# Optimization experiments

Measured on AMD Instinct MI355X. Metric: run time of the kernel, lower is better.

Reference implementation:

```python
import jax, jax.numpy as jnp
import numpy as np

CHEB_K = 3
DIM_IN = 2
HIDDEN = 64
EMBED_DIM = 10
NODE_NUM = 2048
BATCH = 32


def _gconv(x, supports, W, b, cheb_k=CHEB_K):
    # Chebyshev graph conv applied directly to x (equivalent to building
    # T_k(A) matrices then applying: T_k(A) x = 2 A T_{k-1}(A) x - T_{k-2}(A) x).
    xs = [x, jnp.einsum('nm,bmc->bnc', supports, x)]
    for _ in range(2, cheb_k):
        xs.append(2.0 * jnp.einsum('nm,bmc->bnc', supports, xs[-1]) - xs[-2])
    x_g = jnp.concatenate(xs, axis=-1)          # [B, N, cheb_k*C]
    return jnp.einsum('bni,io->bno', x_g, W) + b


def setup_inputs() -> dict:
    key = jax.random.key(0)
    ks = jax.random.split(key, 7)
    c_in = DIM_IN + HIDDEN                       # 66
    # xavier_normal-ish scale for weights
    def xavier(k, fan_in, fan_out):
        std = float(np.sqrt(2.0 / (fan_in + fan_out)))
        return jax.random.normal(k, (fan_in, fan_out), dtype=jnp.float32) * std
    return {
        'x': jax.random.normal(ks[0], (BATCH, NODE_NUM, DIM_IN), dtype=jnp.float32),
        'state': jax.random.normal(ks[1], (BATCH, NODE_NUM, HIDDEN), dtype=jnp.float32),
        'node_embeddings': jax.random.normal(ks[2], (NODE_NUM, EMBED_DIM), dtype=jnp.float32),
        'W_gate': xavier(ks[3], CHEB_K * c_in, 2 * HIDDEN),
        'b_gate': jnp.zeros((2 * HIDDEN,), dtype=jnp.float32),
        'W_update': xavier(ks[4], CHEB_K * c_in, HIDDEN),
        'b_update': jnp.zeros((HIDDEN,), dtype=jnp.float32),
    }


def reference(x, state, node_embeddings, W_gate, b_gate, W_update, b_update):
    # adaptive adjacency: softmax(relu(E E^T), axis=1)
    logits = jnp.einsum('nc,mc->nm', node_embeddings, node_embeddings)
    supports = jax.nn.softmax(jax.nn.relu(logits), axis=1)   # [N, N]

    input_and_state = jnp.concatenate([x, state], axis=-1)   # [B, N, dim_in+hidden]
    z_r = jax.nn.sigmoid(_gconv(input_and_state, supports, W_gate, b_gate))
    z, r = jnp.split(z_r, 2, axis=-1)                        # each [B, N, hidden]
    candidate = jnp.concatenate([x, z * state], axis=-1)
    hc = jnp.tanh(_gconv(candidate, supports, W_update, b_update))
    h = r * state + (1.0 - r) * hc
    return h
```

## Files before the change

### kernel.cpp

```cpp
#include <hip/hip_runtime.h>


typedef __bf16 bf16x8 __attribute__((ext_vector_type(8)));
typedef __bf16 bf16x4 __attribute__((ext_vector_type(4)));
typedef float  f32x4  __attribute__((ext_vector_type(4)));

#define GLB(p) ((__attribute__((address_space(1))) void*)(void*)(p))
#define LDS(p) ((__attribute__((address_space(3))) void*)(p))

__global__ void supports_kernel(const float* __restrict__ E, __bf16* __restrict__ S) {
    const int n = blockIdx.x;
    const int t = threadIdx.x;
    const int l = t & 63, w = t >> 6;
    float en[10];
#pragma unroll
    for (int i = 0; i < 10; ++i) en[i] = E[n * 10 + i];
    float vals[8];
    float mx = 0.f;
#pragma unroll
    for (int q = 0; q < 8; ++q) {
        const int m = q * 256 + t;
        const float* em = E + (size_t)m * 10;
        float d = 0.f;
#pragma unroll
        for (int i = 0; i < 10; ++i) d += en[i] * em[i];
        d = fmaxf(d, 0.f);
        vals[q] = d;
        mx = fmaxf(mx, d);
    }
#pragma unroll
    for (int off = 32; off; off >>= 1) mx = fmaxf(mx, __shfl_xor(mx, off));
    __shared__ float sm[4], ss[4];
    if (l == 0) sm[w] = mx;
    __syncthreads();
    mx = fmaxf(fmaxf(sm[0], sm[1]), fmaxf(sm[2], sm[3]));
    float sum = 0.f;
#pragma unroll
    for (int q = 0; q < 8; ++q) { vals[q] = __expf(vals[q] - mx); sum += vals[q]; }
#pragma unroll
    for (int off = 32; off; off >>= 1) sum += __shfl_xor(sum, off);
    if (l == 0) ss[w] = sum;
    __syncthreads();
    sum = ss[0] + ss[1] + ss[2] + ss[3];
    const float inv = 1.f / sum;
#pragma unroll
    for (int q = 0; q < 8; ++q) S[(size_t)n * 2048 + q * 256 + t] = (__bf16)(vals[q] * inv);
}

__global__ __launch_bounds__(256, 2)
void build_t2(const float* __restrict__ x, const float* __restrict__ st,
              const __bf16* __restrict__ zr, __bf16* __restrict__ T) {
    __shared__ float Ls[66 * 129];
    const int b  = blockIdx.x >> 4;
    const int n0 = (blockIdx.x & 15) << 7;
    const int t = threadIdx.x;
    const size_t mb = (size_t)b * 2048 + n0;
    if (t < 128) {
        const float2 v = *(const float2*)&x[(mb + t) * 2];
        Ls[t] = v.x;
        Ls[129 + t] = v.y;
    }
#pragma unroll
    for (int r = 0; r < 8; ++r) {
        const int task = r * 256 + t;
        const int q = task & 15, n = task >> 4;
        f32x4 v = *(const f32x4*)&st[(mb + n) * 64 + q * 4];
        if (zr) {
            const bf16x4 z = *(const bf16x4*)&zr[(mb + n) * 128 + q * 4];
#pragma unroll
            for (int j = 0; j < 4; ++j) v[j] *= (float)z[j];
        }
        const int base = (2 + q * 4) * 129 + n;
#pragma unroll
        for (int j = 0; j < 4; ++j) Ls[base + j * 129] = v[j];
    }
    __syncthreads();
#pragma unroll
    for (int r = 0; r < 5; ++r) {
        const int task = r * 256 + t;
        if (task < 1056) {
            const int c = task >> 4, seg = task & 15;
            const float* src = &Ls[c * 129 + seg * 8];
            bf16x8 o;
#pragma unroll
            for (int j = 0; j < 8; ++j) o[j] = (__bf16)src[j];
            *(bf16x8*)&T[(size_t)(b * 66 + c) * 2048 + n0 + seg * 8] = o;
        }
    }
}

__global__ __launch_bounds__(256, 2)
void transpose_g(const __bf16* __restrict__ T0, const __bf16* __restrict__ T1,
                 const __bf16* __restrict__ T2, __bf16* __restrict__ G) {
    __shared__ __bf16 Ls[128 * 256];
    const int b  = blockIdx.x >> 4;
    const int n0 = (blockIdx.x & 15) << 7;
    const int t = threadIdx.x;
#pragma unroll
    for (int r = 0; r < 16; ++r) {
        const int task = r * 256 + t;
        const int k = task >> 4, seg = task & 15;
        bf16x8 v;
        if (k < 198) {
            const __bf16* T; int c;
            if (k < 66)       { T = T0; c = k; }
            else if (k < 132) { T = T1; c = k - 66; }
            else              { T = T2; c = k - 132; }
            v = *(const bf16x8*)&T[(size_t)(b * 66 + c) * 2048 + n0 + seg * 8];
        } else {
#pragma unroll
            for (int j = 0; j < 8; ++j) v[j] = (__bf16)0.f;
        }
        const int base = seg * 8 * 256 + (((k >> 3) ^ seg) << 3) + (k & 7);
#pragma unroll
        for (int j = 0; j < 8; ++j) Ls[base + j * 256] = v[j];
    }
    __syncthreads();
#pragma unroll
    for (int r = 0; r < 16; ++r) {
        const int task = r * 256 + t;
        const int m = task >> 5, c8 = task & 31;
        bf16x8 w = *(const bf16x8*)&Ls[m * 256 + ((c8 ^ (m >> 3)) << 3)];
        *(bf16x8*)&G[(size_t)(b * 2048 + n0 + m) * 256 + c8 * 8] = w;
    }
}

__global__ void build_wt(const float* __restrict__ W, __bf16* __restrict__ WT, int Nout) {
    const int id = blockIdx.x * 256 + threadIdx.x;
    const int o = id >> 8, k = id & 255;
    WT[id] = (o < Nout && k < 198) ? (__bf16)W[(size_t)k * Nout + o] : (__bf16)0.f;
}

__global__ __launch_bounds__(256, 3)
void gemm_pipe(const __bf16* __restrict__ A, int lda,
               const __bf16* __restrict__ Bt, int ldb,
               int K, int epi, int swz,
               __bf16* __restrict__ outT, const __bf16* __restrict__ subT,
               float* __restrict__ outF, const float* __restrict__ bias,
               __bf16* __restrict__ zrO, const __bf16* __restrict__ zrI,
               const float* __restrict__ state) {
    __shared__ __align__(16) __bf16 As[2][128 * 64];
    __shared__ __align__(16) __bf16 Bs[2][64 * 64];
    int mt, ct;
    if (swz) { mt = blockIdx.x & 15; ct = blockIdx.x >> 4; }
    else     { mt = blockIdx.x;      ct = blockIdx.y; }
    const int m0 = mt * 128, c0 = ct * 64;
    const int t = threadIdx.x;
    const int l = t & 63, w = t >> 6;
    const int wr = w >> 1, wc = w & 1;
    const int lm = l & 15, kq = l >> 4, lm7 = lm & 7;
    const int sr = l >> 3;
    const int gsw = (l & 7) ^ sr;

    f32x4 acc[4][2];
#pragma unroll
    for (int i = 0; i < 4; ++i)
#pragma unroll
        for (int j = 0; j < 2; ++j) acc[i][j] = (f32x4)0.f;

    const __bf16* Asrc = A  + (size_t)(m0 + w * 8 + sr) * lda + gsw * 8;
    const __bf16* Bsrc = Bt + (size_t)(c0 + w * 8 + sr) * ldb + gsw * 8;
    const int dstA = w * 512 + l * 8;
    const int dstB = w * 512 + l * 8;

    auto stage = [&](int buf, int k0) {
#pragma unroll
        for (int q = 0; q < 4; ++q)
            __builtin_amdgcn_global_load_lds(GLB(Asrc + (size_t)q * 32 * lda + k0),
                                             LDS(&As[buf][q * 2048 + dstA]), 16, 0, 0);
#pragma unroll
        for (int q = 0; q < 2; ++q)
            __builtin_amdgcn_global_load_lds(GLB(Bsrc + (size_t)q * 32 * ldb + k0),
                                             LDS(&Bs[buf][q * 2048 + dstB]), 16, 0, 0);
    };
    auto compute = [&](int buf) {
#pragma unroll
        for (int ks = 0; ks < 2; ++ks) {
            const int ga = (((ks << 2) | kq) ^ lm7) << 3;
            bf16x8 af[4], bfr[2];
#pragma unroll
            for (int i = 0; i < 4; ++i)
                af[i] = *(const bf16x8*)&As[buf][(wr * 64 + i * 16 + lm) * 64 + ga];
#pragma unroll
            for (int j = 0; j < 2; ++j)
                bfr[j] = *(const bf16x8*)&Bs[buf][(wc * 32 + j * 16 + lm) * 64 + ga];
#pragma unroll
            for (int i = 0; i < 4; ++i)
#pragma unroll
                for (int j = 0; j < 2; ++j)
                    acc[i][j] = __builtin_amdgcn_mfma_f32_16x16x32_bf16(af[i], bfr[j], acc[i][j], 0, 0, 0);
        }
    };

    stage(0, 0);
    const int iters = K >> 6;
    for (int i = 0; i + 2 <= iters; i += 2) {
        stage(1, (i + 1) << 6);
        __builtin_amdgcn_sched_barrier(0);
        __builtin_amdgcn_s_waitcnt(0x0F76);
        __builtin_amdgcn_s_barrier();
        __builtin_amdgcn_sched_barrier(0);
        compute(0);
        __builtin_amdgcn_sched_barrier(0);
        __builtin_amdgcn_s_barrier();
        __builtin_amdgcn_sched_barrier(0);
        if (i + 2 < iters) {
            stage(0, (i + 2) << 6);
            __builtin_amdgcn_sched_barrier(0);
            __builtin_amdgcn_s_waitcnt(0x0F76);
        } else {
            __builtin_amdgcn_s_waitcnt(0x0F70);
        }
        __builtin_amdgcn_s_barrier();
        __builtin_amdgcn_sched_barrier(0);
        compute(1);
        __builtin_amdgcn_sched_barrier(0);
        if (i + 4 <= iters) {
            __builtin_amdgcn_s_barrier();
            __builtin_amdgcn_sched_barrier(0);
        }
    }

    const int rb0 = m0 + wr * 64 + kq * 4;
    const int cb0 = c0 + wc * 32 + lm;
#pragma unroll
    for (int i = 0; i < 4; ++i) {
        const int rbase = rb0 + i * 16;
#pragma unroll
        for (int j = 0; j < 2; ++j) {
            const int c = cb0 + j * 16;
            f32x4 v = acc[i][j];
            if (epi == 0) {
                bf16x4 pk;
#pragma unroll
                for (int r = 0; r < 4; ++r) pk[r] = (__bf16)v[r];
                *(bf16x4*)&outT[(size_t)c * 2048 + rbase] = pk;
            } else if (epi == 1) {
                bf16x4 s = *(const bf16x4*)&subT[(size_t)c * 2048 + rbase];
                bf16x4 pk;
#pragma unroll
                for (int r = 0; r < 4; ++r) pk[r] = (__bf16)(2.f * v[r] - (float)s[r]);
                *(bf16x4*)&outT[(size_t)c * 2048 + rbase] = pk;
            } else if (epi == 2) {
                const float bb = bias[c];
#pragma unroll
                for (int r = 0; r < 4; ++r) {
                    float xx = fminf(fmaxf(v[r] + bb, -30.f), 30.f);
                    zrO[(size_t)(rbase + r) * 128 + c] = (__bf16)(1.f / (1.f + __expf(-xx)));
                }
            } else {
                if (c < 64) {
                    const float bb = bias[c];
#pragma unroll
                    for (int r = 0; r < 4; ++r) {
                        const int m = rbase + r;
                        float xx = fminf(fmaxf(v[r] + bb, -15.f), 15.f);
                        float e = __expf(2.f * xx);
                        float hc = (e - 1.f) / (e + 1.f);
                        float rr = (float)zrI[(size_t)m * 128 + 64 + c];
                        float s = state[(size_t)m * 64 + c];
                        outF[(size_t)m * 64 + c] = rr * s + (1.f - rr) * hc;
                    }
                }
            }
        }
    }
}

extern "C" void kernel_launch(void* const* d_in, const int* in_sizes, int n_in,
                              void* d_out, int out_size, void* d_ws, size_t ws_size,
                              hipStream_t stream) {
    (void)in_sizes; (void)n_in; (void)out_size; (void)ws_size;
    const float* x  = (const float*)d_in[0];
    const float* st = (const float*)d_in[1];
    const float* E  = (const float*)d_in[2];
    const float* Wg = (const float*)d_in[3];
    const float* bg = (const float*)d_in[4];
    const float* Wu = (const float*)d_in[5];
    const float* bu = (const float*)d_in[6];
    float* out = (float*)d_out;

    char* p = (char*)d_ws;
    __bf16* S   = (__bf16*)p; p += (size_t)2048 * 2048 * 2;
    __bf16* T0  = (__bf16*)p; p += (size_t)2112 * 2048 * 2;
    __bf16* T1  = (__bf16*)p; p += (size_t)2112 * 2048 * 2;
    __bf16* T2  = (__bf16*)p; p += (size_t)2112 * 2048 * 2;
    __bf16* G   = (__bf16*)p; p += (size_t)65536 * 256 * 2;
    __bf16* ZR  = (__bf16*)p; p += (size_t)65536 * 128 * 2;
    __bf16* WTg = (__bf16*)p; p += 128 * 256 * 2;
    __bf16* WTu = (__bf16*)p; p += 128 * 256 * 2;

    build_wt<<<128, 256, 0, stream>>>(Wg, WTg, 128);
    build_wt<<<128, 256, 0, stream>>>(Wu, WTu, 64);
    supports_kernel<<<2048, 256, 0, stream>>>(E, S);

    build_t2<<<512, 256, 0, stream>>>(x, st, nullptr, T0);
    gemm_pipe<<<528, 256, 0, stream>>>(S, 2048, T0, 2048, 2048, 0, 1, T1, nullptr, nullptr, nullptr, nullptr, nullptr, nullptr);
    gemm_pipe<<<528, 256, 0, stream>>>(S, 2048, T1, 2048, 2048, 1, 1, T2, T0, nullptr, nullptr, nullptr, nullptr, nullptr);
    transpose_g<<<512, 256, 0, stream>>>(T0, T1, T2, G);
    gemm_pipe<<<dim3(512, 2), 256, 0, stream>>>(G, 256, WTg, 256, 256, 2, 0, nullptr, nullptr, nullptr, bg, ZR, nullptr, nullptr);

    build_t2<<<512, 256, 0, stream>>>(x, st, ZR, T0);
    gemm_pipe<<<528, 256, 0, stream>>>(S, 2048, T0, 2048, 2048, 0, 1, T1, nullptr, nullptr, nullptr, nullptr, nullptr, nullptr);
    gemm_pipe<<<528, 256, 0, stream>>>(S, 2048, T1, 2048, 2048, 1, 1, T2, T0, nullptr, nullptr, nullptr, nullptr, nullptr);
    transpose_g<<<512, 256, 0, stream>>>(T0, T1, T2, G);
    gemm_pipe<<<dim3(512, 1), 256, 0, stream>>>(G, 256, WTu, 256, 256, 3, 0, nullptr, nullptr, out, bu, nullptr, ZR, st);
}
```

Measured before the change: 278.6 us.

## Write G directly from build_t2 and GEMM epilogues, drop transpose, triple-buffer GEMM

Removes the separate transpose_g kernel and T2 buffer. build_t2 and the Chebyshev GEMM epilogues now write their outputs straight into the node-major G matrix, using a padded 72-column section layout, and the weight transpose is remapped to match that layout. The goal is to avoid an extra full read and write pass over T0/T1/T2 and two kernel launches per gconv. The GEMM pipeline also moves from double to triple buffering with prefetch distance two, which uses more LDS and lowers launch bounds occupancy from 3 to 2. The new epilogue G stores are scalar and strided, so writes are less coalesced.

```diff
diff --git a/kernel.cpp b/kernel.cpp
--- a/kernel.cpp
+++ b/kernel.cpp
@@ -49,7 +49,8 @@
 
 __global__ __launch_bounds__(256, 2)
 void build_t2(const float* __restrict__ x, const float* __restrict__ st,
-              const __bf16* __restrict__ zr, __bf16* __restrict__ T) {
+              const __bf16* __restrict__ zr, __bf16* __restrict__ T,
+              __bf16* __restrict__ G) {
     __shared__ float Ls[66 * 129];
     const int b  = blockIdx.x >> 4;
     const int n0 = (blockIdx.x & 15) << 7;
@@ -87,60 +88,41 @@
             *(bf16x8*)&T[(size_t)(b * 66 + c) * 2048 + n0 + seg * 8] = o;
         }
     }
-}
-
-__global__ __launch_bounds__(256, 2)
-void transpose_g(const __bf16* __restrict__ T0, const __bf16* __restrict__ T1,
-                 const __bf16* __restrict__ T2, __bf16* __restrict__ G) {
-    __shared__ __bf16 Ls[128 * 256];
-    const int b  = blockIdx.x >> 4;
-    const int n0 = (blockIdx.x & 15) << 7;
-    const int t = threadIdx.x;
-#pragma unroll
-    for (int r = 0; r < 16; ++r) {
-        const int task = r * 256 + t;
-        const int k = task >> 4, seg = task & 15;
-        bf16x8 v;
-        if (k < 198) {
-            const __bf16* T; int c;
-            if (k < 66)       { T = T0; c = k; }
-            else if (k < 132) { T = T1; c = k - 66; }
-            else              { T = T2; c = k - 132; }
-            v = *(const bf16x8*)&T[(size_t)(b * 66 + c) * 2048 + n0 + seg * 8];
-        } else {
-#pragma unroll
-            for (int j = 0; j < 8; ++j) v[j] = (__bf16)0.f;
-        }
-        const int base = seg * 8 * 256 + (((k >> 3) ^ seg) << 3) + (k & 7);
-#pragma unroll
-        for (int j = 0; j < 8; ++j) Ls[base + j * 256] = v[j];
-    }
-    __syncthreads();
-#pragma unroll
-    for (int r = 0; r < 16; ++r) {
-        const int task = r * 256 + t;
-        const int m = task >> 5, c8 = task & 31;
-        bf16x8 w = *(const bf16x8*)&Ls[m * 256 + ((c8 ^ (m >> 3)) << 3)];
-        *(bf16x8*)&G[(size_t)(b * 2048 + n0 + m) * 256 + c8 * 8] = w;
+    {
+        const int n = t & 127, half = t >> 7;
+        const size_t grow = ((size_t)(b * 2048 + n0 + n)) * 256;
+        for (int oct = half * 5; oct < (half ? 9 : 5); ++oct) {
+            bf16x8 o8;
+#pragma unroll
+            for (int j = 0; j < 8; ++j) {
+                const int cc = oct * 8 + j;
+                o8[j] = (cc < 66) ? (__bf16)Ls[cc * 129 + n] : (__bf16)0.f;
+            }
+            *(bf16x8*)&G[grow + oct * 8] = o8;
+        }
     }
 }
 
 __global__ void build_wt(const float* __restrict__ W, __bf16* __restrict__ WT, int Nout) {
     const int id = blockIdx.x * 256 + threadIdx.x;
     const int o = id >> 8, k = id & 255;
-    WT[id] = (o < Nout && k < 198) ? (__bf16)W[(size_t)k * Nout + o] : (__bf16)0.f;
-}
-
-__global__ __launch_bounds__(256, 3)
+    const int jj = (k >= 144) ? 2 : (k >= 72 ? 1 : 0);
+    const int cc = k - 72 * jj;
+    const bool ok = (o < Nout) && (cc < 66) && (k < 216);
+    WT[id] = ok ? (__bf16)W[(size_t)(66 * jj + cc) * Nout + o] : (__bf16)0.f;
+}
+
+__global__ __launch_bounds__(256, 2)
 void gemm_pipe(const __bf16* __restrict__ A, int lda,
                const __bf16* __restrict__ Bt, int ldb,
                int K, int epi, int swz,
                __bf16* __restrict__ outT, const __bf16* __restrict__ subT,
                float* __restrict__ outF, const float* __restrict__ bias,
                __bf16* __restrict__ zrO, const __bf16* __restrict__ zrI,
-               const float* __restrict__ state) {
-    __shared__ __align__(16) __bf16 As[2][128 * 64];
-    __shared__ __align__(16) __bf16 Bs[2][64 * 64];
+               const float* __restrict__ state,
+               __bf16* __restrict__ Gout, int gsec) {
+    __shared__ __align__(16) __bf16 As[3][128 * 64];
+    __shared__ __align__(16) __bf16 Bs[3][64 * 64];
     int mt, ct;
     if (swz) { mt = blockIdx.x & 15; ct = blockIdx.x >> 4; }
     else     { mt = blockIdx.x;      ct = blockIdx.y; }
@@ -161,7 +143,6 @@
     const __bf16* Asrc = A  + (size_t)(m0 + w * 8 + sr) * lda + gsw * 8;
     const __bf16* Bsrc = Bt + (size_t)(c0 + w * 8 + sr) * ldb + gsw * 8;
     const int dstA = w * 512 + l * 8;
-    const int dstB = w * 512 + l * 8;
 
     auto stage = [&](int buf, int k0) {
 #pragma unroll
@@ -171,19 +152,21 @@
 #pragma unroll
         for (int q = 0; q < 2; ++q)
             __builtin_amdgcn_global_load_lds(GLB(Bsrc + (size_t)q * 32 * ldb + k0),
-                                             LDS(&Bs[buf][q * 2048 + dstB]), 16, 0, 0);
+                                             LDS(&Bs[buf][q * 2048 + dstA]), 16, 0, 0);
     };
     auto compute = [&](int buf) {
+        const __bf16* Ab = &As[buf][0];
+        const __bf16* Bb = &Bs[buf][0];
 #pragma unroll
         for (int ks = 0; ks < 2; ++ks) {
             const int ga = (((ks << 2) | kq) ^ lm7) << 3;
             bf16x8 af[4], bfr[2];
 #pragma unroll
             for (int i = 0; i < 4; ++i)
-                af[i] = *(const bf16x8*)&As[buf][(wr * 64 + i * 16 + lm) * 64 + ga];
+                af[i] = *(const bf16x8*)&Ab[(wr * 64 + i * 16 + lm) * 64 + ga];
 #pragma unroll
             for (int j = 0; j < 2; ++j)
-                bfr[j] = *(const bf16x8*)&Bs[buf][(wc * 32 + j * 16 + lm) * 64 + ga];
+                bfr[j] = *(const bf16x8*)&Bb[(wc * 32 + j * 16 + lm) * 64 + ga];
 #pragma unroll
             for (int i = 0; i < 4; ++i)
 #pragma unroll
@@ -193,33 +176,32 @@
     };
 
     stage(0, 0);
+    stage(1, 64);
     const int iters = K >> 6;
-    for (int i = 0; i + 2 <= iters; i += 2) {
-        stage(1, (i + 1) << 6);
-        __builtin_amdgcn_sched_barrier(0);
-        __builtin_amdgcn_s_waitcnt(0x0F76);
+    int cur = 0;
+    for (int it = 0; it < iters - 2; ++it) {
+        int pre = cur + 2; if (pre >= 3) pre -= 3;
+        stage(pre, (it + 2) << 6);
+        __builtin_amdgcn_sched_barrier(0);
+        __builtin_amdgcn_s_waitcnt(0x0F7C);
         __builtin_amdgcn_s_barrier();
         __builtin_amdgcn_sched_barrier(0);
-        compute(0);
+        compute(cur);
         __builtin_amdgcn_sched_barrier(0);
         __builtin_amdgcn_s_barrier();
         __builtin_amdgcn_sched_barrier(0);
-        if (i + 2 < iters) {
-            stage(0, (i + 2) << 6);
-            __builtin_amdgcn_sched_barrier(0);
-            __builtin_amdgcn_s_waitcnt(0x0F76);
-        } else {
-            __builtin_amdgcn_s_waitcnt(0x0F70);
-        }
-        __builtin_amdgcn_s_barrier();
-        __builtin_amdgcn_sched_barrier(0);
-        compute(1);
-        __builtin_amdgcn_sched_barrier(0);
-        if (i + 4 <= iters) {
-            __builtin_amdgcn_s_barrier();
-            __builtin_amdgcn_sched_barrier(0);
-        }
-    }
+        cur = (cur == 2) ? 0 : cur + 1;
+    }
+    __builtin_amdgcn_s_waitcnt(0x0F76);
+    __builtin_amdgcn_s_barrier();
+    __builtin_amdgcn_sched_barrier(0);
+    compute(cur);
+    cur = (cur == 2) ? 0 : cur + 1;
+    __builtin_amdgcn_sched_barrier(0);
+    __builtin_amdgcn_s_waitcnt(0x0F70);
+    __builtin_amdgcn_s_barrier();
+    __builtin_amdgcn_sched_barrier(0);
+    compute(cur);
 
     const int rb0 = m0 + wr * 64 + kq * 4;
     const int cb0 = c0 + wc * 32 + lm;
@@ -230,17 +212,21 @@
         for (int j = 0; j < 2; ++j) {
             const int c = cb0 + j * 16;
             f32x4 v = acc[i][j];
-            if (epi == 0) {
+            if (epi <= 1) {
                 bf16x4 pk;
-#pragma unroll
-                for (int r = 0; r < 4; ++r) pk[r] = (__bf16)v[r];
-                *(bf16x4*)&outT[(size_t)c * 2048 + rbase] = pk;
-            } else if (epi == 1) {
-                bf16x4 s = *(const bf16x4*)&subT[(size_t)c * 2048 + rbase];
-                bf16x4 pk;
-#pragma unroll
-                for (int r = 0; r < 4; ++r) pk[r] = (__bf16)(2.f * v[r] - (float)s[r]);
-                *(bf16x4*)&outT[(size_t)c * 2048 + rbase] = pk;
+                if (epi == 0) {
+#pragma unroll
+                    for (int r = 0; r < 4; ++r) pk[r] = (__bf16)v[r];
+                    *(bf16x4*)&outT[(size_t)c * 2048 + rbase] = pk;
+                } else {
+                    bf16x4 s = *(const bf16x4*)&subT[(size_t)c * 2048 + rbase];
+#pragma unroll
+                    for (int r = 0; r < 4; ++r) pk[r] = (__bf16)(2.f * v[r] - (float)s[r]);
+                }
+                const int b = c / 66, cc = c - b * 66;
+                const size_t gb = ((size_t)(b * 2048 + rbase)) * 256 + gsec + cc;
+#pragma unroll
+                for (int r = 0; r < 4; ++r) Gout[gb + (size_t)r * 256] = pk[r];
             } else if (epi == 2) {
                 const float bb = bias[c];
 #pragma unroll
@@ -284,7 +270,6 @@
     __bf16* S   = (__bf16*)p; p += (size_t)2048 * 2048 * 2;
     __bf16* T0  = (__bf16*)p; p += (size_t)2112 * 2048 * 2;
     __bf16* T1  = (__bf16*)p; p += (size_t)2112 * 2048 * 2;
-    __bf16* T2  = (__bf16*)p; p += (size_t)2112 * 2048 * 2;
     __bf16* G   = (__bf16*)p; p += (size_t)65536 * 256 * 2;
     __bf16* ZR  = (__bf16*)p; p += (size_t)65536 * 128 * 2;
     __bf16* WTg = (__bf16*)p; p += 128 * 256 * 2;
@@ -294,15 +279,13 @@
     build_wt<<<128, 256, 0, stream>>>(Wu, WTu, 64);
     supports_kernel<<<2048, 256, 0, stream>>>(E, S);
 
-    build_t2<<<512, 256, 0, stream>>>(x, st, nullptr, T0);
-    gemm_pipe<<<528, 256, 0, stream>>>(S, 2048, T0, 2048, 2048, 0, 1, T1, nullptr, nullptr, nullptr, nullptr, nullptr, nullptr);
-    gemm_pipe<<<528, 256, 0, stream>>>(S, 2048, T1, 2048, 2048, 1, 1, T2, T0, nullptr, nullptr, nullptr, nullptr, nullptr);
-    transpose_g<<<512, 256, 0, stream>>>(T0, T1, T2, G);
-    gemm_pipe<<<dim3(512, 2), 256, 0, stream>>>(G, 256, WTg, 256, 256, 2, 0, nullptr, nullptr, nullptr, bg, ZR, nullptr, nullptr);
-
-    build_t2<<<512, 256, 0, stream>>>(x, st, ZR, T0);
-    gemm_pipe<<<528, 256, 0, stream>>>(S, 2048, T0, 2048, 2048, 0, 1, T1, nullptr, nullptr, nullptr, nullptr, nullptr, nullptr);
-    gemm_pipe<<<528, 256, 0, stream>>>(S, 2048, T1, 2048, 2048, 1, 1, T2, T0, nullptr, nullptr, nullptr, nullptr, nullptr);
-    transpose_g<<<512, 256, 0, stream>>>(T0, T1, T2, G);
-    gemm_pipe<<<dim3(512, 1), 256, 0, stream>>>(G, 256, WTu, 256, 256, 3, 0, nullptr, nullptr, out, bu, nullptr, ZR, st);
-}
+    build_t2<<<512, 256, 0, stream>>>(x, st, nullptr, T0, G);
+    gemm_pipe<<<528, 256, 0, stream>>>(S, 2048, T0, 2048, 2048, 0, 1, T1, nullptr, nullptr, nullptr, nullptr, nullptr, nullptr, G, 72);
+    gemm_pipe<<<528, 256, 0, stream>>>(S, 2048, T1, 2048, 2048, 1, 1, nullptr, T0, nullptr, nullptr, nullptr, nullptr, nullptr, G, 144);
+    gemm_pipe<<<dim3(512, 2), 256, 0, stream>>>(G, 256, WTg, 256, 256, 2, 0, nullptr, nullptr, nullptr, bg, ZR, nullptr, nullptr, nullptr, 0);
+
+    build_t2<<<512, 256, 0, stream>>>(x, st, ZR, T0, G);
+    gemm_pipe<<<528, 256, 0, stream>>>(S, 2048, T0, 2048, 2048, 0, 1, T1, nullptr, nullptr, nullptr, nullptr, nullptr, nullptr, G, 72);
+    gemm_pipe<<<528, 256, 0, stream>>>(S, 2048, T1, 2048, 2048, 1, 1, nullptr, T0, nullptr, nullptr, nullptr, nullptr, nullptr, G, 144);
+    gemm_pipe<<<dim3(512, 1), 256, 0, stream>>>(G, 256, WTu, 256, 256, 3, 0, nullptr, nullptr, out, bu, nullptr, ZR, st, nullptr, 0);
+}
```

Result: slower. 361.2 us (+29.7%).
